# Optimization experiments

Hardware: AMD Instinct MI355X
Metric: run time of the kernel (lower is better)

## Reference

```python
import jax, jax.numpy as jnp
import numpy as np

N, E = 25000, 100000
V_IN, V_OUT, E_IN, HID = 32, 64, 16, 128
H = 8
C = V_OUT // H  # per-head channels


def _glorot(key, shape, fan_in, fan_out):
    s = jnp.sqrt(6.0 / (fan_in + fan_out))
    return jax.random.uniform(key, shape, minval=-s, maxval=s, dtype=jnp.float32)


def setup_inputs() -> dict:
    key = jax.random.key(0)
    ks = jax.random.split(key, 8)
    x = jax.random.normal(ks[0], (N, V_IN), dtype=jnp.float32)
    e = jax.random.normal(ks[1], (E, E_IN), dtype=jnp.float32)
    e_idx = jax.random.randint(ks[2], (2, E), 0, N, dtype=jnp.int32)
    # edge MLP: Linear(E_IN, HID) -> ReLU -> Linear(HID, V_IN*V_OUT)
    W1 = _glorot(ks[3], (E_IN, HID), E_IN, HID)
    b1 = jnp.zeros((HID,), jnp.float32)
    W2 = _glorot(ks[4], (HID, V_IN * V_OUT), HID, V_IN * V_OUT)
    b2 = jnp.zeros((V_IN * V_OUT,), jnp.float32)
    att = _glorot(ks[5], (1, H, 2 * C), 2 * C, 2 * C)  # pyg glorot on [1,H,2C]
    bias = jnp.zeros((V_OUT,), jnp.float32)            # pyg zeros init
    root = _glorot(ks[6], (V_IN, V_OUT), V_IN, V_OUT)  # NNConv root weight
    return {"x": x, "e_idx": e_idx, "e": e, "W1": W1, "b1": b1,
            "W2": W2, "b2": b2, "att": att, "bias": bias, "root": root}


def reference(x, e_idx, e, W1, b1, W2, b2, att, bias, root):
    src, dst = e_idx[0], e_idx[1]  # source j -> target i (PyG flow)
    # per-edge weight matrices from edge MLP: [E, V_IN, V_OUT]
    w = (jax.nn.relu(e @ W1 + b1) @ W2 + b2).reshape(E, V_IN, V_OUT)
    # gather + per-edge matmul, split into heads: [E, H, C]
    xj = jnp.einsum('ei,eio->eo', x[src], w).reshape(E, H, C)
    xi = jnp.einsum('ei,eio->eo', x[dst], w).reshape(E, H, C)
    # attention logits: (cat([x_i, x_j], -1) * att).sum(-1) -> [E, H]
    alpha = (xi * att[:, :, :C]).sum(-1) + (xj * att[:, :, C:]).sum(-1)
    alpha = jax.nn.leaky_relu(alpha, negative_slope=0.2)
    # segment softmax over incoming edges of each target node
    m = jax.ops.segment_max(alpha, dst, num_segments=N)
    ea = jnp.exp(alpha - m[dst])
    s = jax.ops.segment_sum(ea, dst, num_segments=N)
    alpha = ea / (s[dst] + 1e-16)
    # message = attended x_j (+ per-edge bias as in source); dropout is eval no-op
    msg = (xj * alpha[..., None]).reshape(E, V_OUT) + bias
    out = jax.ops.segment_sum(msg, dst, num_segments=N)  # aggr='add'
    out = out + x @ root + bias  # NNConv root weight + forward bias
    return jax.nn.elu(out)  # wrapper: ELU; dropout no-op in eval
```

## Files before the change

kernel.cpp:

```cpp
#include <hip/hip_runtime.h>
#include <hip/hip_bf16.h>

#define N_NODES 25000
#define N_EDGES 100000
#define E_PAD   100032
#define NSCB    98

typedef __attribute__((ext_vector_type(8))) short bf16x8;
typedef __attribute__((ext_vector_type(4))) float f32x4;

__device__ __forceinline__ unsigned short f2bf(float v) {
  __hip_bfloat16 hb = __float2bfloat16(v);
  return *reinterpret_cast<unsigned short*>(&hb);
}
__device__ __forceinline__ float bf2f(unsigned short u) {
  return __uint_as_float(((unsigned)u) << 16);
}

__global__ __launch_bounds__(256) void k_pre(const float* __restrict__ x,
    const float* __restrict__ root, const float* __restrict__ b2,
    const float* __restrict__ att, const float* __restrict__ bias,
    const float* __restrict__ W2, unsigned char* __restrict__ w2pk,
    float* __restrict__ out, float* __restrict__ xb,
    float* __restrict__ ab1, float* __restrict__ ab2,
    unsigned* __restrict__ deg, unsigned* __restrict__ cnt) {
  __shared__ float lxb[4][64];
  int b = blockIdx.x;
  if (b < 128) {
    int g = b * 256 + threadIdx.x;
    int lane = g & 63, s = (g >> 6) & 3, w = (g >> 8) & 3, i = g >> 10;
    int col = i * 64 + w * 16 + (lane & 15);
    int k0 = s * 32 + (lane >> 4) * 8;
    bf16x8 v;
    #pragma unroll
    for (int j = 0; j < 8; ++j)
      v[j] = (short)f2bf(W2[(size_t)(k0 + j) * 2048 + col]);
    *(bf16x8*)(w2pk + (size_t)g * 16) = v;
    return;
  }
  int g = (b - 128) * 256 + threadIdx.x;
  int n = g >> 6, o = g & 63;
  const float* xr = x + (size_t)n * 32;
  float ra = bias[o], xa = 0.f;
  #pragma unroll
  for (int i = 0; i < 32; ++i) {
    float xv = xr[i];
    ra += xv * root[i * 64 + o];
    xa += xv * b2[i * 64 + o];
  }
  out[g] = ra;
  xb[g] = xa;
  if (o == 0) deg[n] = 0u;
  if (o == 1) cnt[n] = 0u;
  int ln = threadIdx.x >> 6;
  lxb[ln][o] = xa;
  __syncthreads();
  if (o < 8) {
    int hd = o;
    float s1 = 0.f, s2 = 0.f;
    #pragma unroll
    for (int c = 0; c < 8; ++c) {
      float v = lxb[ln][hd * 8 + c];
      s1 += v * att[hd * 16 + c];
      s2 += v * att[hd * 16 + 8 + c];
    }
    size_t idx = (size_t)n * 8 + hd;
    ab1[idx] = s1; ab2[idx] = s2;
  }
}

__global__ __launch_bounds__(256)
__attribute__((amdgpu_waves_per_eu(2)))
void k_main(
    const float* __restrict__ x, const int* __restrict__ ei,
    const float* __restrict__ ef, const float* __restrict__ W1,
    const float* __restrict__ b1,
    const float* __restrict__ att, const float* __restrict__ ab1,
    const float* __restrict__ ab2,
    const unsigned char* __restrict__ w2pk,
    unsigned short* __restrict__ xj_out, float* __restrict__ alpha_out,
    unsigned* __restrict__ deg) {
  __shared__ unsigned char lds_h[16384];
  __shared__ float lds_xs[32 * 64];
  __shared__ float lds_xd[32 * 64];
  const int tid = threadIdx.x;
  const int lane = tid & 63;
  const int w = tid >> 6;
  const int e0 = blockIdx.x * 64;
  const int* srcp = ei;
  const int* dstp = ei + N_EDGES;

  {
    const int l15 = lane & 15;
    const int k0 = (lane >> 4) * 8;
    bf16x8 ha[4], hb[2];
    #pragma unroll
    for (int mt = 0; mt < 4; ++mt) {
      int e = e0 + mt * 16 + l15;
      if (e >= N_EDGES) e = N_EDGES - 1;
      bf16x8 v;
      if (k0 < 16) {
        const float* ap = ef + (size_t)e * 16 + k0;
        f32x4 a0 = *(const f32x4*)(ap);
        f32x4 a1 = *(const f32x4*)(ap + 4);
        #pragma unroll
        for (int t = 0; t < 4; ++t) {
          v[t]     = (short)f2bf(a0[t]);
          v[t + 4] = (short)f2bf(a1[t]);
        }
      } else {
        #pragma unroll
        for (int t = 0; t < 8; ++t) v[t] = 0;
      }
      ha[mt] = v;
    }
    #pragma unroll
    for (int nt = 0; nt < 2; ++nt) {
      int col = w * 32 + nt * 16 + l15;
      bf16x8 v;
      if (k0 < 16) {
        #pragma unroll
        for (int j = 0; j < 8; ++j)
          v[j] = (short)f2bf(W1[(k0 + j) * 128 + col]);
      } else {
        #pragma unroll
        for (int j = 0; j < 8; ++j) v[j] = 0;
      }
      hb[nt] = v;
    }
    const int lpb = (lane >> 4) * 4;
    const int byt = (lane & 7) * 2;
    #pragma unroll
    for (int nt = 0; nt < 2; ++nt) {
      float bv = b1[w * 32 + nt * 16 + l15];
      const int hi = (nt * 2 + (l15 >> 3)) << 4;
      #pragma unroll
      for (int mt = 0; mt < 4; ++mt) {
        f32x4 acc = {bv, bv, bv, bv};
        acc = __builtin_amdgcn_mfma_f32_16x16x32_bf16(ha[mt], hb[nt], acc, 0, 0, 0);
        unsigned base = (unsigned)(mt * 4 + w) * 1024u + (unsigned)hi * 16u + (unsigned)byt;
        #pragma unroll
        for (int r = 0; r < 4; ++r) {
          float hv = acc[r] > 0.f ? acc[r] : 0.f;
          *(unsigned short*)(lds_h + base + (lpb + r) * 16) = f2bf(hv);
        }
      }
    }
  }

  {
    int m = tid & 63;
    int half = (tid >> 6) & 1;
    int which = tid >> 7;
    int eIdx = e0 + m; if (eIdx >= N_EDGES) eIdx = N_EDGES - 1;
    int node = which ? dstp[eIdx] : srcp[eIdx];
    const f32x4* xr = (const f32x4*)(x + (size_t)node * 32 + half * 16);
    float* lx = which ? lds_xd : lds_xs;
    #pragma unroll
    for (int q = 0; q < 4; ++q) {
      f32x4 vv = xr[q];
      int i0 = half * 16 + q * 4;
      #pragma unroll
      for (int j = 0; j < 4; ++j) lx[(i0 + j) * 64 + m] = vv[j];
    }
  }
  __syncthreads();

  const unsigned char* bgp = w2pk + (size_t)w * 4096 + (size_t)lane * 16;
  f32x4 xj_acc[4] = {};
  f32x4 xi_acc[4] = {};
  const int rg4 = ((lane >> 4) & 3) * 4;
  const int lb16 = lane * 16;

  #pragma unroll 1
  for (int p = 0; p < 16; ++p) {
    const int i = 2 * p;
    bf16x8 bA[4], bB[4];
    #pragma unroll
    for (int s = 0; s < 4; ++s) {
      bA[s] = *(const bf16x8*)(bgp + (size_t)i * 16384 + s * 1024);
      bB[s] = *(const bf16x8*)(bgp + (size_t)(i + 1) * 16384 + s * 1024);
    }
    #pragma unroll
    for (int mt = 0; mt < 4; ++mt) {
      f32x4 gA = {0.f, 0.f, 0.f, 0.f};
      f32x4 gB = {0.f, 0.f, 0.f, 0.f};
      #pragma unroll
      for (int s = 0; s < 4; ++s) {
        bf16x8 a = *(const bf16x8*)(lds_h + (mt * 4 + s) * 1024 + lb16);
        gA = __builtin_amdgcn_mfma_f32_16x16x32_bf16(a, bA[s], gA, 0, 0, 0);
        gB = __builtin_amdgcn_mfma_f32_16x16x32_bf16(a, bB[s], gB, 0, 0, 0);
      }
      f32x4 xsv0 = *(const f32x4*)(lds_xs + i * 64 + mt * 16 + rg4);
      f32x4 xdv0 = *(const f32x4*)(lds_xd + i * 64 + mt * 16 + rg4);
      f32x4 xsv1 = *(const f32x4*)(lds_xs + (i + 1) * 64 + mt * 16 + rg4);
      f32x4 xdv1 = *(const f32x4*)(lds_xd + (i + 1) * 64 + mt * 16 + rg4);
      #pragma unroll
      for (int r = 0; r < 4; ++r) {
        xj_acc[mt][r] += xsv0[r] * gA[r] + xsv1[r] * gB[r];
        xi_acc[mt][r] += xdv0[r] * gA[r] + xdv1[r] * gB[r];
      }
    }
  }

  const int h2 = (lane >> 3) & 1;
  const int cc = lane & 7;
  const int head = 2 * w + h2;
  const float a1v = att[head * 16 + cc];
  const float a2v = att[head * 16 + 8 + cc];
  #pragma unroll
  for (int mt = 0; mt < 4; ++mt) {
    #pragma unroll
    for (int r = 0; r < 4; ++r) {
      int row = mt * 16 + rg4 + r;
      int eIdx = e0 + row;
      xj_out[(size_t)eIdx * 64 + w * 16 + (lane & 15)] = f2bf(xj_acc[mt][r]);
      float v = xi_acc[mt][r] * a1v + xj_acc[mt][r] * a2v;
      v += __shfl_xor(v, 1);
      v += __shfl_xor(v, 2);
      v += __shfl_xor(v, 4);
      if (cc == 0 && eIdx < N_EDGES) {
        int d = dstp[eIdx];
        float lg = v + ab1[(size_t)d * 8 + head] + ab2[(size_t)srcp[eIdx] * 8 + head];
        lg = lg > 0.f ? lg : 0.2f * lg;
        alpha_out[(size_t)eIdx * 8 + head] = lg;
        if (w == 0 && (lane & 15) == 0) atomicAdd(deg + d, 1u);
      }
    }
  }
}

__global__ __launch_bounds__(256) void k_scan1(const unsigned* __restrict__ deg,
    unsigned* __restrict__ off, unsigned* __restrict__ bsum) {
  __shared__ unsigned sd[256];
  int tid = threadIdx.x;
  int n = blockIdx.x * 256 + tid;
  unsigned v = (n < N_NODES) ? deg[n] : 0u;
  sd[tid] = v;
  __syncthreads();
  #pragma unroll
  for (int ofs = 1; ofs < 256; ofs <<= 1) {
    unsigned t = (tid >= ofs) ? sd[tid - ofs] : 0u;
    __syncthreads();
    sd[tid] += t;
    __syncthreads();
  }
  if (n < N_NODES) off[n] = sd[tid] - v;
  if (tid == 255) bsum[blockIdx.x] = sd[255];
}

__global__ void k_scan2(unsigned* __restrict__ bsum) {
  if (threadIdx.x == 0 && blockIdx.x == 0) {
    unsigned run = 0;
    for (int i = 0; i < NSCB; ++i) { unsigned t = bsum[i]; bsum[i] = run; run += t; }
  }
}

__global__ __launch_bounds__(256) void k_fill(const int* __restrict__ ei,
    const unsigned* __restrict__ off, const unsigned* __restrict__ bsum,
    unsigned* __restrict__ cnt, unsigned* __restrict__ elist) {
  int e = blockIdx.x * 256 + threadIdx.x;
  if (e >= N_EDGES) return;
  int d = ei[N_EDGES + e];
  unsigned pos = off[d] + bsum[d >> 8] + atomicAdd(cnt + d, 1u);
  elist[pos] = (unsigned)e;
}

__global__ __launch_bounds__(256) void k_agg(const unsigned* __restrict__ off,
    const unsigned* __restrict__ bsum, const unsigned* __restrict__ deg,
    const unsigned* __restrict__ elist, const float* __restrict__ alpha,
    const unsigned short* __restrict__ xj, const float* __restrict__ bias,
    float* __restrict__ out) {
  int g = blockIdx.x * 256 + threadIdx.x;
  int n = g >> 6, o = g & 63, hd = o >> 3;
  unsigned base = off[n] + bsum[n >> 8];
  unsigned dg = deg[n];
  float m = -1e30f;
  for (unsigned j = 0; j < dg; ++j) {
    unsigned e = elist[base + j];
    m = fmaxf(m, alpha[(size_t)e * 8 + hd]);
  }
  float s = 0.f, acc = 0.f;
  for (unsigned j = 0; j < dg; ++j) {
    unsigned e = elist[base + j];
    float p = expf(alpha[(size_t)e * 8 + hd] - m);
    s += p;
    acc += p * bf2f(xj[(size_t)e * 64 + o]);
  }
  float val = out[g] + acc / (s + 1e-16f) + (float)dg * bias[o];
  out[g] = val > 0.f ? val : expm1f(val);
}

extern "C" void kernel_launch(void* const* d_in, const int* in_sizes, int n_in,
                              void* d_out, int out_size, void* d_ws, size_t ws_size,
                              hipStream_t stream) {
  const float* x    = (const float*)d_in[0];
  const int*   eidx = (const int*)d_in[1];
  const float* ef   = (const float*)d_in[2];
  const float* W1   = (const float*)d_in[3];
  const float* b1   = (const float*)d_in[4];
  const float* W2   = (const float*)d_in[5];
  const float* b2   = (const float*)d_in[6];
  const float* att  = (const float*)d_in[7];
  const float* bias = (const float*)d_in[8];
  const float* root = (const float*)d_in[9];
  float* out = (float*)d_out;
  char* ws = (char*)d_ws;

  unsigned char* w2pk = (unsigned char*)(ws + 0);
  float* xb    = (float*)(ws + 524288);
  float* ab1   = (float*)(ws + 6924288);
  float* ab2   = (float*)(ws + 7724288);
  unsigned short* xj_ws = (unsigned short*)(ws + 8524288);
  float* al_ws = (float*)(ws + 21328384);
  unsigned* deg   = (unsigned*)(ws + 24529408);
  unsigned* off   = (unsigned*)(ws + 24629760);
  unsigned* bsum  = (unsigned*)(ws + 24730112);
  unsigned* cnt   = (unsigned*)(ws + 24730624);
  unsigned* elist = (unsigned*)(ws + 24830976);

  k_pre  <<<128 + N_NODES * 64 / 256, 256, 0, stream>>>(x, root, b2, att, bias,
                                                  W2, w2pk, out, xb, ab1, ab2, deg, cnt);
  k_main <<<E_PAD / 64, 256, 0, stream>>>(x, eidx, ef, W1, b1, att, ab1, ab2,
                                          w2pk, xj_ws, al_ws, deg);
  k_scan1<<<NSCB, 256, 0, stream>>>(deg, off, bsum);
  k_scan2<<<1, 64, 0, stream>>>(bsum);
  k_fill <<<(N_EDGES + 255) / 256, 256, 0, stream>>>(eidx, off, bsum, cnt, elist);
  k_agg  <<<N_NODES * 64 / 256, 256, 0, stream>>>(off, bsum, deg, elist, al_ws,
                                                  xj_ws, bias, out);
}
```

Baseline: 151.7 us.

## Merge scan kernels via atomic block base and move degree count into pre-pass

Degree counting moves out of k_main into extra blocks of k_pre, and the counters are now zeroed with a memset. The two-pass scan (k_scan1 plus a serial single-thread k_scan2) becomes one kernel that reserves each block's base offset with an atomicAdd on a global counter. k_fill bumps the offsets directly with atomics, so the separate cnt array goes away, and k_agg rebuilds each node's start as off minus deg. This removes a kernel launch and a serial loop, at the cost of a memset call and CSR order that now depends on which scan block wins its atomic, which still gives a valid CSR.

New measurement: 151.1 us, median of 3. No clear change (-0.4%).

```diff
diff --git a/kernel.cpp b/kernel.cpp
--- a/kernel.cpp
+++ b/kernel.cpp
@@ -5,6 +5,7 @@
 #define N_EDGES 100000
 #define E_PAD   100032
 #define NSCB    98
+#define NHB     391
 
 typedef __attribute__((ext_vector_type(8))) short bf16x8;
 typedef __attribute__((ext_vector_type(4))) float f32x4;
@@ -20,10 +21,11 @@
 __global__ __launch_bounds__(256) void k_pre(const float* __restrict__ x,
     const float* __restrict__ root, const float* __restrict__ b2,
     const float* __restrict__ att, const float* __restrict__ bias,
-    const float* __restrict__ W2, unsigned char* __restrict__ w2pk,
+    const float* __restrict__ W2, const int* __restrict__ ei,
+    unsigned char* __restrict__ w2pk,
     float* __restrict__ out, float* __restrict__ xb,
     float* __restrict__ ab1, float* __restrict__ ab2,
-    unsigned* __restrict__ deg, unsigned* __restrict__ cnt) {
+    unsigned* __restrict__ deg) {
   __shared__ float lxb[4][64];
   int b = blockIdx.x;
   if (b < 128) {
@@ -36,6 +38,11 @@
     for (int j = 0; j < 8; ++j)
       v[j] = (short)f2bf(W2[(size_t)(k0 + j) * 2048 + col]);
     *(bf16x8*)(w2pk + (size_t)g * 16) = v;
+    return;
+  }
+  if (b >= 128 + 6250) {
+    int e = (b - 128 - 6250) * 256 + threadIdx.x;
+    if (e < N_EDGES) atomicAdd(deg + ei[N_EDGES + e], 1u);
     return;
   }
   int g = (b - 128) * 256 + threadIdx.x;
@@ -50,8 +57,6 @@
   }
   out[g] = ra;
   xb[g] = xa;
-  if (o == 0) deg[n] = 0u;
-  if (o == 1) cnt[n] = 0u;
   int ln = threadIdx.x >> 6;
   lxb[ln][o] = xa;
   __syncthreads();
@@ -78,8 +83,7 @@
     const float* __restrict__ att, const float* __restrict__ ab1,
     const float* __restrict__ ab2,
     const unsigned char* __restrict__ w2pk,
-    unsigned short* __restrict__ xj_out, float* __restrict__ alpha_out,
-    unsigned* __restrict__ deg) {
+    unsigned short* __restrict__ xj_out, float* __restrict__ alpha_out) {
   __shared__ unsigned char lds_h[16384];
   __shared__ float lds_xs[32 * 64];
   __shared__ float lds_xd[32 * 64];
@@ -224,15 +228,15 @@
         float lg = v + ab1[(size_t)d * 8 + head] + ab2[(size_t)srcp[eIdx] * 8 + head];
         lg = lg > 0.f ? lg : 0.2f * lg;
         alpha_out[(size_t)eIdx * 8 + head] = lg;
-        if (w == 0 && (lane & 15) == 0) atomicAdd(deg + d, 1u);
-      }
-    }
-  }
-}
-
-__global__ __launch_bounds__(256) void k_scan1(const unsigned* __restrict__ deg,
-    unsigned* __restrict__ off, unsigned* __restrict__ bsum) {
+      }
+    }
+  }
+}
+
+__global__ __launch_bounds__(256) void k_scan(const unsigned* __restrict__ deg,
+    unsigned* __restrict__ off, unsigned* __restrict__ gbase) {
   __shared__ unsigned sd[256];
+  __shared__ unsigned blockbase;
   int tid = threadIdx.x;
   int n = blockIdx.x * 256 + tid;
   unsigned v = (n < N_NODES) ? deg[n] : 0u;
@@ -245,36 +249,29 @@
     sd[tid] += t;
     __syncthreads();
   }
-  if (n < N_NODES) off[n] = sd[tid] - v;
-  if (tid == 255) bsum[blockIdx.x] = sd[255];
-}
-
-__global__ void k_scan2(unsigned* __restrict__ bsum) {
-  if (threadIdx.x == 0 && blockIdx.x == 0) {
-    unsigned run = 0;
-    for (int i = 0; i < NSCB; ++i) { unsigned t = bsum[i]; bsum[i] = run; run += t; }
-  }
+  if (tid == 255) blockbase = atomicAdd(gbase, sd[255]);
+  __syncthreads();
+  if (n < N_NODES) off[n] = blockbase + sd[tid] - v;
 }
 
 __global__ __launch_bounds__(256) void k_fill(const int* __restrict__ ei,
-    const unsigned* __restrict__ off, const unsigned* __restrict__ bsum,
-    unsigned* __restrict__ cnt, unsigned* __restrict__ elist) {
+    unsigned* __restrict__ off, unsigned* __restrict__ elist) {
   int e = blockIdx.x * 256 + threadIdx.x;
   if (e >= N_EDGES) return;
   int d = ei[N_EDGES + e];
-  unsigned pos = off[d] + bsum[d >> 8] + atomicAdd(cnt + d, 1u);
+  unsigned pos = atomicAdd(off + d, 1u);
   elist[pos] = (unsigned)e;
 }
 
 __global__ __launch_bounds__(256) void k_agg(const unsigned* __restrict__ off,
-    const unsigned* __restrict__ bsum, const unsigned* __restrict__ deg,
+    const unsigned* __restrict__ deg,
     const unsigned* __restrict__ elist, const float* __restrict__ alpha,
     const unsigned short* __restrict__ xj, const float* __restrict__ bias,
     float* __restrict__ out) {
   int g = blockIdx.x * 256 + threadIdx.x;
   int n = g >> 6, o = g & 63, hd = o >> 3;
-  unsigned base = off[n] + bsum[n >> 8];
   unsigned dg = deg[n];
+  unsigned base = off[n] - dg;
   float m = -1e30f;
   for (unsigned j = 0; j < dg; ++j) {
     unsigned e = elist[base + j];
@@ -314,18 +311,17 @@
   unsigned short* xj_ws = (unsigned short*)(ws + 8524288);
   float* al_ws = (float*)(ws + 21328384);
   unsigned* deg   = (unsigned*)(ws + 24529408);
-  unsigned* off   = (unsigned*)(ws + 24629760);
-  unsigned* bsum  = (unsigned*)(ws + 24730112);
-  unsigned* cnt   = (unsigned*)(ws + 24730624);
-  unsigned* elist = (unsigned*)(ws + 24830976);
-
-  k_pre  <<<128 + N_NODES * 64 / 256, 256, 0, stream>>>(x, root, b2, att, bias,
-                                                  W2, w2pk, out, xb, ab1, ab2, deg, cnt);
+  unsigned* gbase = (unsigned*)(ws + 24629760);
+  unsigned* off   = (unsigned*)(ws + 24630016);
+  unsigned* elist = (unsigned*)(ws + 24730368);
+
+  hipMemsetAsync(deg, 0, 100352 + 256, stream);
+  k_pre  <<<128 + 6250 + NHB, 256, 0, stream>>>(x, root, b2, att, bias,
+                                                W2, eidx, w2pk, out, xb, ab1, ab2, deg);
   k_main <<<E_PAD / 64, 256, 0, stream>>>(x, eidx, ef, W1, b1, att, ab1, ab2,
-                                          w2pk, xj_ws, al_ws, deg);
-  k_scan1<<<NSCB, 256, 0, stream>>>(deg, off, bsum);
-  k_scan2<<<1, 64, 0, stream>>>(bsum);
-  k_fill <<<(N_EDGES + 255) / 256, 256, 0, stream>>>(eidx, off, bsum, cnt, elist);
-  k_agg  <<<N_NODES * 64 / 256, 256, 0, stream>>>(off, bsum, deg, elist, al_ws,
+                                          w2pk, xj_ws, al_ws);
+  k_scan <<<NSCB, 256, 0, stream>>>(deg, off, gbase);
+  k_fill <<<NHB, 256, 0, stream>>>(eidx, off, elist);
+  k_agg  <<<N_NODES * 64 / 256, 256, 0, stream>>>(off, deg, elist, al_ws,
                                                   xj_ws, bias, out);
 }
```
